# Kernel optimization log

Hardware: AMD Instinct MI355X
Metric: run time of the kernel (lower is better)

## Reference

```python
import jax, jax.numpy as jnp
import numpy as np

B, S, H, NH, HD = 2, 2048, 1024, 16, 64
RD = 16            # rotary_dim = head_dim * 0.25
W = 16             # mini_context_length (sliding window)
SCALE = HD ** -0.5
ROPE_BASE = 10000.0


def setup_inputs() -> dict:
    key = jax.random.key(0)
    ks = jax.random.split(key, 10)
    p = lambda k, shape: (jax.random.normal(k, shape, dtype=jnp.float32) * 0.02)
    return {
        "hidden_states": jax.random.normal(ks[0], (B, S, H), dtype=jnp.float32),
        "Wqkv": p(ks[1], (3 * H, H)), "bqkv": p(ks[2], (3 * H,)),
        "Wqa": p(ks[3], (H, H)),      "bqa": p(ks[4], (H,)),
        "Wka": p(ks[5], (H, H)),      "bka": p(ks[6], (H,)),
        "Wd": p(ks[7], (H, H)),       "bd": p(ks[8], (H,)),
    }


def _rotate_half(x):
    x1, x2 = jnp.split(x, 2, axis=-1)
    return jnp.concatenate([-x2, x1], axis=-1)


def _apply_rope(q, k, seq_len):
    # GPT-NeoX style rotary on the first RD dims. q,k: [B,NH,S,RD]
    inv_freq = 1.0 / (ROPE_BASE ** (jnp.arange(0, RD, 2, dtype=jnp.float32) / RD))
    t = jnp.arange(seq_len, dtype=jnp.float32)
    freqs = jnp.outer(t, inv_freq)                     # [S, RD//2]
    emb = jnp.concatenate([freqs, freqs], axis=-1)     # [S, RD]
    cos = jnp.cos(emb)[None, None]                      # [1,1,S,RD]
    sin = jnp.sin(emb)[None, None]
    return q * cos + _rotate_half(q) * sin, k * cos + _rotate_half(k) * sin


def reference(hidden_states, Wqkv, bqkv, Wqa, bqa, Wka, bka, Wd, bd):
    b, s, _ = hidden_states.shape
    qkv = hidden_states @ Wqkv.T + bqkv                       # [B,S,3H]
    qkv = qkv.reshape(b, s, 3, NH, HD).transpose(2, 0, 3, 1, 4)
    q, k, v = qkv[0], qkv[1], qkv[2]                          # [B,NH,S,HD]

    q_rot, k_rot = _apply_rope(q[..., :RD], k[..., :RD], s)
    q = jnp.concatenate([q_rot, q[..., RD:]], axis=-1)
    k = jnp.concatenate([k_rot, k[..., RD:]], axis=-1)

    # ----- Stage 1: sliding-window local attention (vectorized) -----
    pos = jnp.arange(s)
    idx = pos[:, None] - (W - 1) + jnp.arange(W)[None, :]     # [S,W]
    valid = idx >= 0
    idxc = jnp.clip(idx, 0, s - 1)
    k_win = k[:, :, idxc, :]                                   # [B,NH,S,W,HD]
    v_win = v[:, :, idxc, :]
    scores = jnp.einsum('bhsd,bhswd->bhsw', q, k_win) * SCALE
    scores = jnp.where(valid[None, None], scores, -jnp.inf)
    probs = jax.nn.softmax(scores, axis=-1)
    A = jnp.einsum('bhsw,bhswd->bhsd', probs, v_win)           # [B,NH,S,HD]

    A_hidden = A.transpose(0, 2, 1, 3).reshape(b, s, H)        # [B,S,H]

    # ----- Stage 2: causal global attention over A -----
    qa = (A_hidden @ Wqa.T + bqa).reshape(b, s, NH, HD).transpose(0, 2, 1, 3)
    ka = (A_hidden @ Wka.T + bka).reshape(b, s, NH, HD).transpose(0, 2, 1, 3)
    g = jnp.einsum('bhqd,bhkd->bhqk', qa, ka) * SCALE          # [B,NH,S,S]
    causal = pos[:, None] >= pos[None, :]
    g = jnp.where(causal[None, None], g, -jnp.inf)
    pg = jax.nn.softmax(g, axis=-1)
    out = jnp.einsum('bhqk,bhkd->bhqd', pg, A)                 # [B,NH,S,HD]
    out = out.transpose(0, 2, 1, 3).reshape(b, s, H)
    return out @ Wd.T + bd
```

## Files before the change

kernel.cpp:

```cpp
#include <hip/hip_runtime.h>
#include <hip/hip_bf16.h>
#include <cstdint>
#include <cstddef>

typedef __bf16 bf16;
typedef __bf16 bf16x4 __attribute__((ext_vector_type(4)));
typedef __bf16 bf16x8 __attribute__((ext_vector_type(8)));
typedef float  f32x4  __attribute__((ext_vector_type(4)));

#define DEVINL __device__ __forceinline__

constexpr int   Bc  = 2, Sc = 2048, Hc = 1024, NHc = 16, HDc = 64;
constexpr int   Tc  = Bc * Sc;
constexpr float L2E = 1.44269504088896340736f;
constexpr float NEG_BIG = -1.0e30f;

typedef __attribute__((address_space(1))) void AS1void;
typedef __attribute__((address_space(3))) void AS3void;

DEVINL void load_lds16(const bf16* g, bf16* l) {
  __builtin_amdgcn_global_load_lds((AS1void*)g, (AS3void*)l, 16, 0, 0);
}


__global__ __launch_bounds__(256)
void convert_all(const float* __restrict__ hs, const float* __restrict__ Wqkv,
                 const float* __restrict__ Wqa, const float* __restrict__ Wka,
                 const float* __restrict__ Wd, const float* __restrict__ bqa,
                 const float* __restrict__ bka,
                 bf16* __restrict__ hsb, bf16* __restrict__ wqkvb,
                 bf16* __restrict__ wqakab, bf16* __restrict__ wdb,
                 float* __restrict__ bqaka) {
  const int blk = blockIdx.x;
  if (blk >= 5120) {
    const int i = threadIdx.x * 8;
    const float* src = (i < 1024) ? (bqa + i) : (bka + i - 1024);
    *(f32x4*)(bqaka + i)     = *(const f32x4*)src;
    *(f32x4*)(bqaka + i + 4) = *(const f32x4*)(src + 4);
    return;
  }
  const float* src; bf16* dst; int base;
  if      (blk < 2048) { src = hs;   dst = hsb;                    base = blk; }
  else if (blk < 3584) { src = Wqkv; dst = wqkvb;                  base = blk - 2048; }
  else if (blk < 4096) { src = Wqa;  dst = wqakab;                 base = blk - 3584; }
  else if (blk < 4608) { src = Wka;  dst = wqakab + 1024 * 1024;   base = blk - 4096; }
  else                 { src = Wd;   dst = wdb;                    base = blk - 4608; }
  const int i = (base * 256 + threadIdx.x) * 8;
  f32x4 a = *(const f32x4*)(src + i);
  f32x4 b = *(const f32x4*)(src + i + 4);
  bf16x8 v;
#pragma unroll
  for (int j = 0; j < 4; j++) { v[j] = (bf16)a[j]; v[4 + j] = (bf16)b[j]; }
  *(bf16x8*)(dst + i) = v;
}

template <typename CT>
__global__ __launch_bounds__(256, 3)
void gemm128(const bf16* __restrict__ A, const bf16* __restrict__ Bw,
             const float* __restrict__ bias, CT* __restrict__ C,
             int M, int N, int K) {
  __shared__ __attribute__((aligned(16))) bf16 As[128 * 64];
  __shared__ __attribute__((aligned(16))) bf16 Bs[128 * 64];

  const int tid = threadIdx.x, wv = tid >> 6, lane = tid & 63;
  const int m0 = blockIdx.y * 128, n0 = blockIdx.x * 128;
  const int col = lane & 15, quad = lane >> 4;
  const int wrow = (wv >> 1) * 64, wcol = (wv & 1) * 64;

  f32x4 acc[4][4];
#pragma unroll
  for (int i = 0; i < 4; i++)
#pragma unroll
    for (int j = 0; j < 4; j++) acc[i][j] = f32x4{0.f, 0.f, 0.f, 0.f};

  const int srow = tid >> 3;
  const int scol = (((tid & 7) ^ (srow & 7)) << 3);
  const bf16* Ag = A  + (size_t)(m0 + srow) * K + scol;
  const bf16* Bg = Bw + (size_t)(n0 + srow) * K + scol;
  const int cs = col & 7;

  for (int k0 = 0; k0 < K; k0 += 64) {
#pragma unroll
    for (int c = 0; c < 4; c++) {
      load_lds16(Ag + (size_t)(c * 32) * K + k0, As + c * 2048 + tid * 8);
      load_lds16(Bg + (size_t)(c * 32) * K + k0, Bs + c * 2048 + tid * 8);
    }
    __syncthreads();
#pragma unroll
    for (int kk = 0; kk < 64; kk += 32) {
      const int so = ((((kk >> 3) + quad) ^ cs) << 3);
      bf16x8 af[4], bfr[4];
#pragma unroll
      for (int i = 0; i < 4; i++)
        af[i] = *(const bf16x8*)(As + (wrow + i * 16 + col) * 64 + so);
#pragma unroll
      for (int j = 0; j < 4; j++)
        bfr[j] = *(const bf16x8*)(Bs + (wcol + j * 16 + col) * 64 + so);
#pragma unroll
      for (int i = 0; i < 4; i++)
#pragma unroll
        for (int j = 0; j < 4; j++)
          acc[i][j] = __builtin_amdgcn_mfma_f32_16x16x32_bf16(af[i], bfr[j], acc[i][j], 0, 0, 0);
    }
    __syncthreads();
  }

#pragma unroll
  for (int j = 0; j < 4; j++) {
    const int c = n0 + wcol + j * 16 + col;
    const float bv = bias[c];
#pragma unroll
    for (int i = 0; i < 4; i++)
#pragma unroll
      for (int r = 0; r < 4; r++) {
        const int rr = m0 + wrow + i * 16 + quad * 4 + r;
        C[(size_t)rr * N + c] = (CT)(acc[i][j][r] + bv);
      }
  }
}

template <typename CT>
__global__ __launch_bounds__(256, 4)
void gemm6464(const bf16* __restrict__ A, const bf16* __restrict__ Bw,
              const float* __restrict__ bias, CT* __restrict__ C,
              int M, int N, int K) {
  __shared__ __attribute__((aligned(16))) bf16 As[64 * 64];
  __shared__ __attribute__((aligned(16))) bf16 Bs[64 * 64];

  const int tid = threadIdx.x, wv = tid >> 6, lane = tid & 63;
  const int m0 = blockIdx.y * 64, n0 = blockIdx.x * 64;
  const int col = lane & 15, quad = lane >> 4;

  f32x4 acc[4];
#pragma unroll
  for (int j = 0; j < 4; j++) acc[j] = f32x4{0.f, 0.f, 0.f, 0.f};

  const int srow = tid >> 3;
  const int scol = (((tid & 7) ^ (srow & 7)) << 3);
  const bf16* Ag = A  + (size_t)(m0 + srow) * K + scol;
  const bf16* Bg = Bw + (size_t)(n0 + srow) * K + scol;
  const int cs = col & 7;

  for (int k0 = 0; k0 < K; k0 += 64) {
#pragma unroll
    for (int c = 0; c < 2; c++) {
      load_lds16(Ag + (size_t)(c * 32) * K + k0, As + c * 2048 + tid * 8);
      load_lds16(Bg + (size_t)(c * 32) * K + k0, Bs + c * 2048 + tid * 8);
    }
    __syncthreads();
#pragma unroll
    for (int kk = 0; kk < 64; kk += 32) {
      const int so = ((((kk >> 3) + quad) ^ cs) << 3);
      bf16x8 af = *(const bf16x8*)(As + (wv * 16 + col) * 64 + so);
#pragma unroll
      for (int j = 0; j < 4; j++) {
        bf16x8 bfr = *(const bf16x8*)(Bs + (j * 16 + col) * 64 + so);
        acc[j] = __builtin_amdgcn_mfma_f32_16x16x32_bf16(af, bfr, acc[j], 0, 0, 0);
      }
    }
    __syncthreads();
  }

#pragma unroll
  for (int j = 0; j < 4; j++) {
    const int c = n0 + j * 16 + col;
    const float bv = bias[c];
#pragma unroll
    for (int r = 0; r < 4; r++) {
      const int rr = m0 + wv * 16 + quad * 4 + r;
      C[(size_t)rr * N + c] = (CT)(acc[j][r] + bv);
    }
  }
}

__global__ __launch_bounds__(256)
void window_attn(const bf16* __restrict__ qkv, bf16* __restrict__ Ah,
                 bf16* __restrict__ VTg) {
  __shared__ __attribute__((aligned(16))) bf16 Kw[31 * 72];
  __shared__ __attribute__((aligned(16))) bf16 Vw[31 * 72];
  const int g  = blockIdx.x;
  const int st = g & 127;
  const int h  = (g >> 7) & 15;
  const int b  = g >> 11;
  const int s0 = st * 16;
  const int tid = threadIdx.x;

  if ((tid < 124) || (tid >= 128 && tid < 252)) {
    const bool isK = tid < 124;
    const int lt  = isK ? tid : tid - 128;
    const int r   = lt >> 2, off = (lt & 3) << 4;
    int sidx = s0 - 15 + r; if (sidx < 0) sidx = 0;
    const bf16* src = qkv + (size_t)(b * Sc + sidx) * 3072 + (isK ? 1024 : 2048) + h * 64 + off;
    bf16x8 v0 = *(const bf16x8*)src;
    bf16x8 v1 = *(const bf16x8*)(src + 8);
    if (isK && off == 0) {
#pragma unroll
      for (int j = 0; j < 8; j++) {
        const float invf = exp2f(-(float)j * 1.66096404744368128f);
        float sn, csn;
        sincosf((float)sidx * invf, &sn, &csn);
        const float x1 = (float)v0[j], x2 = (float)v1[j];
        v0[j] = (bf16)(x1 * csn - x2 * sn);
        v1[j] = (bf16)(x2 * csn + x1 * sn);
      }
    }
    bf16* dst = (isK ? Kw : Vw) + r * 72 + off;
    *(bf16x8*)dst       = v0;
    *(bf16x8*)(dst + 8) = v1;
  }
  __syncthreads();

  const int wv = tid >> 6, lane = tid & 63;
  const int subq = lane >> 4, lane16 = lane & 15;
  const int s = s0 + wv * 4 + subq;
  const int t = b * Sc + s;
  const int d0 = lane16 * 4;

  float qd[4];
  {
    bf16x4 qv = *(const bf16x4*)(qkv + (size_t)t * 3072 + h * 64 + d0);
#pragma unroll
    for (int j = 0; j < 4; j++) qd[j] = (float)qv[j];
  }
  float pd[4];
#pragma unroll
  for (int j = 0; j < 4; j++) pd[j] = __shfl_xor(qd[j], 2, 64);
  if (lane16 < 4) {
#pragma unroll
    for (int j = 0; j < 4; j++) {
      const int jabs = d0 + j;
      const float invf = exp2f(-(float)(jabs & 7) * 1.66096404744368128f);
      float sn, csn;
      sincosf((float)s * invf, &sn, &csn);
      qd[j] = (jabs < 8) ? (qd[j] * csn - pd[j] * sn) : (qd[j] * csn + pd[j] * sn);
    }
  }

  float sc[16];
#pragma unroll
  for (int w = 0; w < 16; w++) {
    const int idxp = s - 15 + w;
    const int row = idxp - s0 + 15;
    bf16x4 kv = *(const bf16x4*)(Kw + row * 72 + d0);
    float p = qd[0] * (float)kv[0] + qd[1] * (float)kv[1] +
              qd[2] * (float)kv[2] + qd[3] * (float)kv[3];
#pragma unroll
    for (int m = 1; m < 16; m <<= 1) p += __shfl_xor(p, m, 64);
    sc[w] = (idxp < 0) ? NEG_BIG : p * 0.125f;
  }
  float mx = sc[0];
#pragma unroll
  for (int w = 1; w < 16; w++) mx = fmaxf(mx, sc[w]);
  float sum = 0.f;
#pragma unroll
  for (int w = 0; w < 16; w++) { sc[w] = exp2f((sc[w] - mx) * L2E); sum += sc[w]; }
  const float inv = 1.0f / fmaxf(sum, 1e-30f);

  float acc[4] = {0.f, 0.f, 0.f, 0.f};
#pragma unroll
  for (int w = 0; w < 16; w++) {
    const int idxp = s - 15 + w;
    const int row = idxp - s0 + 15;
    bf16x4 vv = *(const bf16x4*)(Vw + row * 72 + d0);
#pragma unroll
    for (int j = 0; j < 4; j++) acc[j] += sc[w] * (float)vv[j];
  }
  bf16x4 ov;
#pragma unroll
  for (int j = 0; j < 4; j++) ov[j] = (bf16)(acc[j] * inv);
  *(bf16x4*)(Ah + (size_t)t * 1024 + h * 64 + d0) = ov;
  bf16* vt = VTg + (((size_t)(b * 16 + h)) * 64 + d0) * 2048 + s;
#pragma unroll
  for (int j = 0; j < 4; j++) vt[(size_t)j * 2048] = ov[j];
}

__global__ __launch_bounds__(256, 3)
void flash_attn(const bf16* __restrict__ Q, const bf16* __restrict__ Kt,
                const bf16* __restrict__ VTg, bf16* __restrict__ O) {
  constexpr int QS = 2048;
  constexpr float SHIFT = 16.0f;
  __shared__ __attribute__((aligned(16))) bf16 K_lds[128 * 64];
  __shared__ __attribute__((aligned(16))) bf16 VT_lds[64 * 128];
  __shared__ __attribute__((aligned(16))) bf16 P_lds[4][16 * 136];

  const int tid = threadIdx.x, wv = tid >> 6, lane = tid & 63;
  const int bh = blockIdx.x;
  const int y  = blockIdx.y;
  const int gq = y & 7, kq = y >> 3;
  const int qt = (kq == 0) ? gq : (kq == 1) ? (15 - gq)
               : (kq == 2) ? (16 + gq) : (31 - gq);
  const int b = bh >> 4, h = bh & 15;
  const int col = lane & 15, quad = lane >> 4;
  const size_t bS = (size_t)b * Sc;
  const int hd = h * 64;

  const int krow = tid >> 3;
  const int kcol = (((tid & 7) ^ (krow & 7)) << 3);
  const int vrow = tid >> 4;
  const int vcol = (((tid & 15) ^ vrow) << 3);
  const int cs8 = col & 7;

  const int qbase = qt * 64 + wv * 16;
  const int nkt = (qt + 2) >> 1;

  const bf16* qptr = Q + (bS + qbase + col) * QS + hd + quad * 8;
  bf16x8 qf[2];
  qf[0] = *(const bf16x8*)qptr;
  qf[1] = *(const bf16x8*)(qptr + 32);
#pragma unroll
  for (int hh = 0; hh < 2; hh++)
#pragma unroll
    for (int j = 0; j < 8; j++) qf[hh][j] = (bf16)((float)qf[hh][j] * 0.125f);

  f32x4 oacc[4];
#pragma unroll
  for (int i = 0; i < 4; i++) oacc[i] = f32x4{0.f, 0.f, 0.f, 0.f};
  float lrow[4] = {0.f, 0.f, 0.f, 0.f};

  for (int kt0 = 0; kt0 < nkt; kt0++) {
    const int k0 = kt0 * 128;
#pragma unroll
    for (int c = 0; c < 4; c++) {
      load_lds16(Kt + (bS + k0 + c * 32 + krow) * QS + hd + kcol,
                 K_lds + c * 2048 + tid * 8);
      load_lds16(VTg + ((size_t)bh * 64 + c * 16 + vrow) * 2048 + k0 + vcol,
                 VT_lds + c * 2048 + tid * 8);
    }
    __syncthreads();

    f32x4 sacc[8];
#pragma unroll
    for (int sub = 0; sub < 8; sub++) {
      f32x4 a = f32x4{0.f, 0.f, 0.f, 0.f};
#pragma unroll
      for (int hh = 0; hh < 2; hh++) {
        const int so = (((hh * 4 + quad) ^ cs8) << 3);
        bf16x8 kf = *(const bf16x8*)(K_lds + (sub * 16 + col) * 64 + so);
        a = __builtin_amdgcn_mfma_f32_16x16x32_bf16(qf[hh], kf, a, 0, 0, 0);
      }
      sacc[sub] = a;
    }
    if (kt0 == nkt - 1) {
#pragma unroll
      for (int sub = 0; sub < 8; sub++)
#pragma unroll
        for (int r = 0; r < 4; r++) {
          const int key = k0 + sub * 16 + col;
          const int qq  = qbase + quad * 4 + r;
          if (key > qq) sacc[sub][r] = NEG_BIG;
        }
    }
#pragma unroll
    for (int sub = 0; sub < 8; sub++)
#pragma unroll
      for (int r = 0; r < 4; r++)
        sacc[sub][r] = exp2f(sacc[sub][r] * L2E - SHIFT);
#pragma unroll
    for (int r = 0; r < 4; r++)
      lrow[r] += ((sacc[0][r] + sacc[1][r]) + (sacc[2][r] + sacc[3][r]))
               + ((sacc[4][r] + sacc[5][r]) + (sacc[6][r] + sacc[7][r]));
#pragma unroll
    for (int sub = 0; sub < 8; sub++)
#pragma unroll
      for (int r = 0; r < 4; r++)
        P_lds[wv][(quad * 4 + r) * 136 + sub * 16 + col] = (bf16)sacc[sub][r];
#pragma unroll
    for (int kk = 0; kk < 128; kk += 32) {
      bf16x8 pf = *(const bf16x8*)&P_lds[wv][col * 136 + kk + quad * 8];
      const int vso = ((((kk >> 3) + quad) ^ col) << 3);
#pragma unroll
      for (int nb = 0; nb < 4; nb++) {
        bf16x8 vf = *(const bf16x8*)(VT_lds + (nb * 16 + col) * 128 + vso);
        oacc[nb] = __builtin_amdgcn_mfma_f32_16x16x32_bf16(pf, vf, oacc[nb], 0, 0, 0);
      }
    }
    __syncthreads();
  }

#pragma unroll
  for (int m = 1; m < 16; m <<= 1)
#pragma unroll
    for (int r = 0; r < 4; r++) lrow[r] += __shfl_xor(lrow[r], m, 64);
#pragma unroll
  for (int r = 0; r < 4; r++) lrow[r] = 1.0f / fmaxf(lrow[r], 1e-37f);
#pragma unroll
  for (int nb = 0; nb < 4; nb++)
#pragma unroll
    for (int r = 0; r < 4; r++) {
      const int qq = qbase + quad * 4 + r;
      O[(bS + qq) * 1024 + hd + nb * 16 + col] = (bf16)(oacc[nb][r] * lrow[r]);
    }
}

extern "C" void kernel_launch(void* const* d_in, const int* in_sizes, int n_in,
                              void* d_out, int out_size, void* d_ws, size_t ws_size,
                              hipStream_t stream) {
  (void)in_sizes; (void)n_in; (void)out_size; (void)ws_size;
  const float* hs   = (const float*)d_in[0];
  const float* Wqkv = (const float*)d_in[1];
  const float* bqkv = (const float*)d_in[2];
  const float* Wqa  = (const float*)d_in[3];
  const float* bqa  = (const float*)d_in[4];
  const float* Wka  = (const float*)d_in[5];
  const float* bka  = (const float*)d_in[6];
  const float* Wd   = (const float*)d_in[7];
  const float* bd   = (const float*)d_in[8];
  float* out = (float*)d_out;

  const size_t TH = (size_t)Tc * Hc;
  bf16* dob   = (bf16*)d_out;
  bf16* hsb   = dob;
  bf16* wqkvb = dob + TH;
  bf16* Ah    = dob;
  bf16* VTg   = dob + TH;
  bf16* ws     = (bf16*)d_ws;
  bf16* qkv    = ws;
  bf16* qaka   = ws;
  bf16* oh     = ws + 2 * TH;
  bf16* wqakab = ws + 3 * TH;
  bf16* wdb    = wqakab + 2 * 1024 * 1024;
  float* bqaka = (float*)(wdb + 1024 * 1024);

  convert_all<<<dim3(5121), 256, 0, stream>>>(hs, Wqkv, Wqa, Wka, Wd, bqa, bka,
                                              hsb, wqkvb, wqakab, wdb, bqaka);

  gemm128<bf16><<<dim3(24, 32), 256, 0, stream>>>(hsb, wqkvb, bqkv, qkv, Tc, 3 * Hc, Hc);
  window_attn<<<dim3(Tc * NHc / 16), 256, 0, stream>>>(qkv, Ah, VTg);
  gemm128<bf16><<<dim3(16, 32), 256, 0, stream>>>(Ah, wqakab, bqaka, qaka, Tc, 2 * Hc, Hc);
  flash_attn<<<dim3(Bc * NHc, 32), 256, 0, stream>>>(qaka, qaka + Hc, VTg, oh);
  gemm6464<float><<<dim3(16, 64), 256, 0, stream>>>(oh, wdb, bd, out, Tc, Hc, Hc);
}
```

Baseline: 241.8 us.

## Keep softmax probabilities in registers via transposed S and permlane swaps

```diff
diff --git a/kernel.cpp b/kernel.cpp
--- a/kernel.cpp
+++ b/kernel.cpp
@@ -274,14 +274,13 @@
   for (int j = 0; j < 4; j++) vt[(size_t)j * 2048] = ov[j];
 }
 
-__global__ __launch_bounds__(256, 3)
+__global__ __launch_bounds__(256, 4)
 void flash_attn(const bf16* __restrict__ Q, const bf16* __restrict__ Kt,
                 const bf16* __restrict__ VTg, bf16* __restrict__ O) {
   constexpr int QS = 2048;
   constexpr float SHIFT = 16.0f;
   __shared__ __attribute__((aligned(16))) bf16 K_lds[128 * 64];
   __shared__ __attribute__((aligned(16))) bf16 VT_lds[64 * 128];
-  __shared__ __attribute__((aligned(16))) bf16 P_lds[4][16 * 136];
 
   const int tid = threadIdx.x, wv = tid >> 6, lane = tid & 63;
   const int bh = blockIdx.x;
@@ -315,7 +314,7 @@
   f32x4 oacc[4];
 #pragma unroll
   for (int i = 0; i < 4; i++) oacc[i] = f32x4{0.f, 0.f, 0.f, 0.f};
-  float lrow[4] = {0.f, 0.f, 0.f, 0.f};
+  float lsum = 0.f;
 
   for (int kt0 = 0; kt0 < nkt; kt0++) {
     const int k0 = kt0 * 128;
@@ -336,53 +335,63 @@
       for (int hh = 0; hh < 2; hh++) {
         const int so = (((hh * 4 + quad) ^ cs8) << 3);
         bf16x8 kf = *(const bf16x8*)(K_lds + (sub * 16 + col) * 64 + so);
-        a = __builtin_amdgcn_mfma_f32_16x16x32_bf16(qf[hh], kf, a, 0, 0, 0);
+        a = __builtin_amdgcn_mfma_f32_16x16x32_bf16(kf, qf[hh], a, 0, 0, 0);
       }
       sacc[sub] = a;
     }
     if (kt0 == nkt - 1) {
+      const int qq = qbase + col;
 #pragma unroll
       for (int sub = 0; sub < 8; sub++)
 #pragma unroll
         for (int r = 0; r < 4; r++) {
-          const int key = k0 + sub * 16 + col;
-          const int qq  = qbase + quad * 4 + r;
+          const int key = k0 + sub * 16 + quad * 4 + r;
           if (key > qq) sacc[sub][r] = NEG_BIG;
         }
     }
 #pragma unroll
     for (int sub = 0; sub < 8; sub++)
 #pragma unroll
-      for (int r = 0; r < 4; r++)
+      for (int r = 0; r < 4; r++) {
         sacc[sub][r] = exp2f(sacc[sub][r] * L2E - SHIFT);
-#pragma unroll
-    for (int r = 0; r < 4; r++)
-      lrow[r] += ((sacc[0][r] + sacc[1][r]) + (sacc[2][r] + sacc[3][r]))
-               + ((sacc[4][r] + sacc[5][r]) + (sacc[6][r] + sacc[7][r]));
-#pragma unroll
-    for (int sub = 0; sub < 8; sub++)
-#pragma unroll
-      for (int r = 0; r < 4; r++)
-        P_lds[wv][(quad * 4 + r) * 136 + sub * 16 + col] = (bf16)sacc[sub][r];
-#pragma unroll
-    for (int kk = 0; kk < 128; kk += 32) {
-      bf16x8 pf = *(const bf16x8*)&P_lds[wv][col * 136 + kk + quad * 8];
-      const int vso = ((((kk >> 3) + quad) ^ col) << 3);
+        lsum += sacc[sub][r];
+      }
+
+#pragma unroll
+    for (int t = 0; t < 4; t++) {
+      uint32_t a0, a1, b0, b1;
+      asm("v_cvt_pk_bf16_f32 %0, %1, %2"
+          : "=v"(a0) : "v"(sacc[2 * t][0]), "v"(sacc[2 * t][1]));
+      asm("v_cvt_pk_bf16_f32 %0, %1, %2"
+          : "=v"(a1) : "v"(sacc[2 * t][2]), "v"(sacc[2 * t][3]));
+      asm("v_cvt_pk_bf16_f32 %0, %1, %2"
+          : "=v"(b0) : "v"(sacc[2 * t + 1][0]), "v"(sacc[2 * t + 1][1]));
+      asm("v_cvt_pk_bf16_f32 %0, %1, %2"
+          : "=v"(b1) : "v"(sacc[2 * t + 1][2]), "v"(sacc[2 * t + 1][3]));
+      asm("v_permlane32_swap_b32 %0, %1" : "+v"(a0), "+v"(b0));
+      asm("v_permlane16_swap_b32 %0, %1" : "+v"(a0), "+v"(b0));
+      asm("v_permlane32_swap_b32 %0, %1" : "+v"(a1), "+v"(b1));
+      asm("v_permlane16_swap_b32 %0, %1" : "+v"(a1), "+v"(b1));
+      union { uint32_t u[4]; bf16x8 v; } pk;
+      pk.u[0] = a0; pk.u[1] = a1; pk.u[2] = b0; pk.u[3] = b1;
+      const int vso = (((4 * t + quad) ^ col) << 3);
 #pragma unroll
       for (int nb = 0; nb < 4; nb++) {
         bf16x8 vf = *(const bf16x8*)(VT_lds + (nb * 16 + col) * 128 + vso);
-        oacc[nb] = __builtin_amdgcn_mfma_f32_16x16x32_bf16(pf, vf, oacc[nb], 0, 0, 0);
-      }
-    }
-    __syncthreads();
-  }
-
-#pragma unroll
-  for (int m = 1; m < 16; m <<= 1)
-#pragma unroll
-    for (int r = 0; r < 4; r++) lrow[r] += __shfl_xor(lrow[r], m, 64);
-#pragma unroll
-  for (int r = 0; r < 4; r++) lrow[r] = 1.0f / fmaxf(lrow[r], 1e-37f);
+        oacc[nb] = __builtin_amdgcn_mfma_f32_16x16x32_bf16(pk.v, vf, oacc[nb], 0, 0, 0);
+      }
+    }
+    __syncthreads();
+  }
+
+  float tot = lsum;
+  tot += __shfl_xor(tot, 16, 64);
+  tot += __shfl_xor(tot, 32, 64);
+  float lrow[4];
+#pragma unroll
+  for (int r = 0; r < 4; r++)
+    lrow[r] = 1.0f / fmaxf(__shfl(tot, quad * 4 + r, 16), 1e-37f);
+
 #pragma unroll
   for (int nb = 0; nb < 4; nb++)
 #pragma unroll
```

Measured after the change: 225.0 us. -6.9%, faster.
